# Optimization experiments

Hardware: AMD Instinct MI355X
Metric: run time of the kernel (lower is better)

## Reference

```python
import jax, jax.numpy as jnp
import numpy as np

N_NODES = 50000
N_EDGES = 800000
IN_CH = 256
OUT_CH = 128


def setup_inputs() -> dict:
    key = jax.random.key(0)
    k1, k2, k3, k4, k5, k6 = jax.random.split(key, 6)
    x = jax.random.normal(k1, (N_NODES, IN_CH), dtype=jnp.float32)
    edge_rows = jax.random.randint(k2, (N_EDGES,), 0, N_NODES, dtype=jnp.int64)
    edge_cols = jax.random.randint(k3, (N_EDGES,), 0, N_NODES, dtype=jnp.int64)
    # positive edge weights, roughly like a normalized adjacency (~1/degree)
    edge_vals = jax.random.uniform(k4, (N_EDGES,), dtype=jnp.float32) / 16.0
    # xavier_uniform: bound = sqrt(6/(fan_in+fan_out))
    bound = float(np.sqrt(6.0 / (IN_CH + OUT_CH)))
    weight = jax.random.uniform(k5, (IN_CH, OUT_CH), dtype=jnp.float32, minval=-bound, maxval=bound)
    gate_weight = jax.random.uniform(k6, (IN_CH, OUT_CH), dtype=jnp.float32, minval=-bound, maxval=bound)
    return {"x": x, "edge_rows": edge_rows, "edge_cols": edge_cols,
            "edge_vals": edge_vals, "weight": weight, "gate_weight": gate_weight}


def _spmm(edge_rows, edge_cols, edge_vals, dense, n_rows):
    # out[r] = sum over edges (r, c, v): v * dense[c]
    gathered = edge_vals[:, None] * dense[edge_cols]  # [E, out_ch]
    return jax.ops.segment_sum(gathered, edge_rows, num_segments=n_rows)


def reference(x, edge_rows, edge_cols, edge_vals, weight, gate_weight):
    support = x @ weight          # [N, out_ch]
    gate = x @ gate_weight        # [N, out_ch]
    n = x.shape[0]
    agg_support = _spmm(edge_rows, edge_cols, edge_vals, support, n)
    agg_gate = _spmm(edge_rows, edge_cols, edge_vals, gate, n)
    return jax.nn.sigmoid(agg_gate) * agg_support
```

## Files before the change

kernel.cpp:

```cpp
#include <hip/hip_runtime.h>
#include <hip/hip_bf16.h>

#define IN_CH 256
#define OUT_CH 128
#define NCAT 256
#define CAP 64
#define RPB 128
#define BINCAP 3072
#define EPB 4096

typedef __attribute__((ext_vector_type(8))) short bf16x8;
typedef __attribute__((ext_vector_type(4))) float f32x4;

__device__ __forceinline__ unsigned short f2bf(float f) {
  unsigned int u = __builtin_bit_cast(unsigned int, f);
  u += 0x7FFFu + ((u >> 16) & 1u);
  return (unsigned short)(u >> 16);
}
__device__ __forceinline__ unsigned int pack2bf(float a, float b) {
  return (unsigned int)f2bf(a) | ((unsigned int)f2bf(b) << 16);
}
__device__ __forceinline__ float bflo(unsigned int u) {
  return __builtin_bit_cast(float, u << 16);
}
__device__ __forceinline__ float bfhi(unsigned int u) {
  return __builtin_bit_cast(float, u & 0xFFFF0000u);
}

__global__ __launch_bounds__(256) void init_wcat(
    const float* __restrict__ w, const float* __restrict__ gw,
    unsigned short* __restrict__ wcat2, int* __restrict__ coarse_cnt,
    int nbins) {
  const int b = blockIdx.x;
  if (b < 256) {
    const int c = b;
    const int k = threadIdx.x;
    const int wc = c >> 6, s = c & 63, n = s >> 4, lr = s & 15;
    const int ch = 32 * wc + (n & 1) * 16 + lr;
    const float v = (n < 2) ? w[(size_t)k * 128 + ch]
                            : gw[(size_t)k * 128 + ch];
    wcat2[(size_t)c * 256 + k] = f2bf(v);
  } else {
    for (int j = threadIdx.x; j < nbins; j += 256) coarse_cnt[j] = 0;
  }
}

#define AST 80

__global__ __launch_bounds__(256) void gemm_and_bin(
    const float* __restrict__ x, const unsigned short* __restrict__ wcat2,
    char* __restrict__ comb, int nrows,
    const int* __restrict__ er, const int* __restrict__ ec,
    const float* __restrict__ ev, int* __restrict__ coarse_cnt,
    unsigned* __restrict__ cA, unsigned char* __restrict__ cB,
    int E, int nbins, int binBlocks) {
  __shared__ char smem[64 * AST + 256 * AST];

  if (blockIdx.x < binBlocks) {
    int* scnt = (int*)smem;
    int* sbase = (int*)smem + 512;
    const int t = threadIdx.x;
    const int e0 = blockIdx.x * EPB;

    for (int j = t; j < 512; j += 256) scnt[j] = 0;
    __syncthreads();

    int myr[16];
#pragma unroll
    for (int i = 0; i < 16; ++i) {
      const int e = e0 + i * 256 + t;
      int r = -1;
      if (e < E) { r = er[e]; atomicAdd(&scnt[r >> 7], 1); }
      myr[i] = r;
    }
    __syncthreads();

    for (int j = t; j < nbins; j += 256)
      sbase[j] = (scnt[j] > 0) ? atomicAdd(&coarse_cnt[j], scnt[j]) : 0;
    __syncthreads();
    for (int j = t; j < 512; j += 256) scnt[j] = 0;
    __syncthreads();

#pragma unroll
    for (int i = 0; i < 16; ++i) {
      const int r = myr[i];
      if (r >= 0) {
        const int e = e0 + i * 256 + t;
        const int b = r >> 7;
        const int idx = sbase[b] + atomicAdd(&scnt[b], 1);
        if (idx < BINCAP) {
          const size_t g = (size_t)b * BINCAP + idx;
          cA[g] = ((unsigned)ec[e] << 16) | (unsigned)f2bf(ev[e]);
          cB[g] = (unsigned char)(r & (RPB - 1));
        }
      }
    }
    return;
  }

  char* As = smem;
  char* Bs = smem + 64 * AST;
  const int t = threadIdx.x;
  const int lane = t & 63;
  const int wc = t >> 6;
  const int lrow = lane & 15;
  const int klane = lane >> 4;
  const int blockRow = (blockIdx.x - binBlocks) * 64;

  f32x4 acc[4][4];
#pragma unroll
  for (int m = 0; m < 4; ++m)
#pragma unroll
    for (int n = 0; n < 4; ++n) acc[m][n] = (f32x4){0.f, 0.f, 0.f, 0.f};

  const int arow = t >> 2;
  const int aseg = t & 3;
  const int agrow = blockRow + arow;
  const bool aok = (agrow < nrows);
  const float* xrow = x + (size_t)agrow * IN_CH + aseg * 8;
  const char* bsrc0 = (const char*)wcat2 + (size_t)t * 512;

  for (int kt = 0; kt < IN_CH; kt += 32) {
    {
      float4 v0 = make_float4(0, 0, 0, 0), v1 = v0;
      if (aok) {
        v0 = *(const float4*)(xrow + kt);
        v1 = *(const float4*)(xrow + kt + 4);
      }
      uint4 pk;
      pk.x = pack2bf(v0.x, v0.y); pk.y = pack2bf(v0.z, v0.w);
      pk.z = pack2bf(v1.x, v1.y); pk.w = pack2bf(v1.z, v1.w);
      *(uint4*)(As + arow * AST + aseg * 16) = pk;
    }
    {
      const char* src = bsrc0 + kt * 2;
      char* dst = Bs + t * AST;
      *(uint4*)(dst + 0)  = *(const uint4*)(src + 0);
      *(uint4*)(dst + 16) = *(const uint4*)(src + 16);
      *(uint4*)(dst + 32) = *(const uint4*)(src + 32);
      *(uint4*)(dst + 48) = *(const uint4*)(src + 48);
    }
    __syncthreads();

    bf16x8 af[4], bfm[4];
#pragma unroll
    for (int m = 0; m < 4; ++m)
      af[m] = *(const bf16x8*)(As + (m * 16 + lrow) * AST + klane * 16);
#pragma unroll
    for (int n = 0; n < 4; ++n)
      bfm[n] = *(const bf16x8*)(Bs + (wc * 64 + n * 16 + lrow) * AST + klane * 16);
#pragma unroll
    for (int m = 0; m < 4; ++m)
#pragma unroll
      for (int n = 0; n < 4; ++n)
        acc[m][n] = __builtin_amdgcn_mfma_f32_16x16x32_bf16(af[m], bfm[n], acc[m][n], 0, 0, 0);
    __syncthreads();
  }

#pragma unroll
  for (int m = 0; m < 4; ++m) {
#pragma unroll
    for (int j = 0; j < 4; ++j) {
      const int grow = blockRow + m * 16 + klane * 4 + j;
      if (grow < nrows) {
        uint2 val;
        val.x = pack2bf(acc[m][0][j], acc[m][2][j]);
        val.y = pack2bf(acc[m][1][j], acc[m][3][j]);
        *(uint2*)(comb + (size_t)grow * 512 + wc * 128 + lrow * 8) = val;
      }
    }
  }
}

__global__ __launch_bounds__(256) void bin_fine(
    const int* __restrict__ coarse_cnt, const unsigned* __restrict__ cA,
    const unsigned char* __restrict__ cB, int* __restrict__ cnt,
    unsigned* __restrict__ bucket4, int nrows) {
  __shared__ unsigned fine[RPB * CAP];
  __shared__ int lcnt[RPB];
  const int t = threadIdx.x;
  const int b = blockIdx.x;
  const int r0 = b * RPB;

  for (int j = t; j < RPB; j += 256) lcnt[j] = 0;
  __syncthreads();

  const int nE = min(coarse_cnt[b], BINCAP);
  for (int i = t; i < nE; i += 256) {
    const unsigned a = cA[(size_t)b * BINCAP + i];
    const int rl = cB[(size_t)b * BINCAP + i];
    const int idx = atomicAdd(&lcnt[rl], 1);
    if (idx < CAP) fine[rl * CAP + idx] = a;
  }
  __syncthreads();

  if (t < RPB && r0 + t < nrows) cnt[r0 + t] = min(lcnt[t], CAP);

  for (int s = t; s < RPB * CAP; s += 256) {
    const int rl = s >> 6;
    const int sl = s & 63;
    if (sl < min(lcnt[rl], CAP) && r0 + rl < nrows)
      bucket4[(size_t)(r0 + rl) * CAP + sl] = fine[s];
  }
}

__global__ __launch_bounds__(256) void spmm_fused(
    const unsigned* __restrict__ bucket4, const int* __restrict__ cnt,
    const char* __restrict__ comb, float* __restrict__ out, int nrows) {
  const int wid = (int)((blockIdx.x * 256 + threadIdx.x) >> 6);
  const int lane = threadIdx.x & 63;
  if (wid >= nrows) return;

  const int deg = min(cnt[wid], CAP);
  float s1 = 0.f, g1 = 0.f, s2 = 0.f, g2 = 0.f;

  if (deg > 0) {
    const unsigned my = bucket4[(size_t)wid * CAP + lane];
    for (int d = 0; d < deg; d += 8) {
      unsigned cj[8]; float vj[8]; uint2 q[8];
#pragma unroll
      for (int j = 0; j < 8; ++j) {
        const int dj = d + j;
        const int ds = dj < deg ? dj : deg - 1;
        const unsigned ent = (unsigned)__shfl((int)my, ds);
        cj[j] = ent >> 16;
        vj[j] = (dj < deg) ? bflo(ent) : 0.f;
      }
#pragma unroll
      for (int j = 0; j < 8; ++j)
        q[j] = *(const uint2*)(comb + (size_t)cj[j] * 512 + lane * 8);
#pragma unroll
      for (int j = 0; j < 8; ++j) {
        s1 += vj[j] * bflo(q[j].x);  g1 += vj[j] * bfhi(q[j].x);
        s2 += vj[j] * bflo(q[j].y);  g2 += vj[j] * bfhi(q[j].y);
      }
    }
  }
  const int gg = lane >> 4, lr = lane & 15;
  const int c1 = 32 * gg + lr;
  const float o1 = s1 / (1.f + __expf(-g1));
  const float o2 = s2 / (1.f + __expf(-g2));
  out[(size_t)wid * OUT_CH + c1]      = o1;
  out[(size_t)wid * OUT_CH + c1 + 16] = o2;
}

extern "C" void kernel_launch(void* const* d_in, const int* in_sizes, int n_in,
                              void* d_out, int out_size, void* d_ws, size_t ws_size,
                              hipStream_t stream) {
  const float* x  = (const float*)d_in[0];
  const int*   er = (const int*)d_in[1];
  const int*   ec = (const int*)d_in[2];
  const float* ev = (const float*)d_in[3];
  const float* w  = (const float*)d_in[4];
  const float* gw = (const float*)d_in[5];
  float* out = (float*)d_out;

  const int N = in_sizes[0] / IN_CH;
  const int E = in_sizes[1];
  const int nbins = (N + RPB - 1) / RPB;

  char* ws = (char*)d_ws;
  char* comb = ws;
  size_t off = (size_t)N * 512;
  unsigned short* wcat2 = (unsigned short*)(ws + off);  off += 256 * 256 * 2;
  int* cnt = (int*)(ws + off);                          off += ((size_t)N * 4 + 255) & ~255ull;
  unsigned* bucket4 = (unsigned*)(ws + off);            off += (size_t)N * CAP * 4;
  int* coarse_cnt = (int*)(ws + off);                   off += ((size_t)nbins * 4 + 255) & ~255ull;
  unsigned* cA = (unsigned*)(ws + off);                 off += (size_t)nbins * BINCAP * 4;
  unsigned char* cB = (unsigned char*)(ws + off);

  init_wcat<<<257, 256, 0, stream>>>(w, gw, wcat2, coarse_cnt, nbins);

  const int binBlocks = (E + EPB - 1) / EPB;
  const int gemmBlocks = (N + 63) / 64;
  gemm_and_bin<<<binBlocks + gemmBlocks, 256, 0, stream>>>(
      x, wcat2, comb, N, er, ec, ev, coarse_cnt, cA, cB, E, nbins, binBlocks);

  bin_fine<<<nbins, 256, 0, stream>>>(coarse_cnt, cA, cB, cnt, bucket4, N);

  const int blocks = (N + 3) / 4;
  spmm_fused<<<blocks, 256, 0, stream>>>(bucket4, cnt, comb, out, N);
}
```

Baseline: 109.7 us.

## Replace global-atomic coarse binning with per-block sorted segments and metadata

Each binning block now counting-sorts its 4096 edges by row bin in shared memory and writes a contiguous segment plus per-bin offset/count metadata, instead of reserving space in global bins with global atomics. The fine-binning kernel gathers each bin's pieces from all binning blocks, using a prefix scan and a binary search to map edge index to its source block. This removes the global atomics, the coarse counter zeroing, and the fixed bin capacity with its overflow drop. In exchange it adds scattered reads across about 196 segments per bin and a hardcoded NBIN that ties the code to the node count.

Measured after the change: 105.3 us. -4.1%, faster.

```diff
diff --git a/kernel.cpp b/kernel.cpp
--- a/kernel.cpp
+++ b/kernel.cpp
@@ -3,11 +3,11 @@
 
 #define IN_CH 256
 #define OUT_CH 128
-#define NCAT 256
 #define CAP 64
 #define RPB 128
-#define BINCAP 3072
 #define EPB 4096
+#define NBIN 392
+#define METAST 400
 
 typedef __attribute__((ext_vector_type(8))) short bf16x8;
 typedef __attribute__((ext_vector_type(4))) float f32x4;
@@ -29,20 +29,14 @@
 
 __global__ __launch_bounds__(256) void init_wcat(
     const float* __restrict__ w, const float* __restrict__ gw,
-    unsigned short* __restrict__ wcat2, int* __restrict__ coarse_cnt,
-    int nbins) {
-  const int b = blockIdx.x;
-  if (b < 256) {
-    const int c = b;
-    const int k = threadIdx.x;
-    const int wc = c >> 6, s = c & 63, n = s >> 4, lr = s & 15;
-    const int ch = 32 * wc + (n & 1) * 16 + lr;
-    const float v = (n < 2) ? w[(size_t)k * 128 + ch]
-                            : gw[(size_t)k * 128 + ch];
-    wcat2[(size_t)c * 256 + k] = f2bf(v);
-  } else {
-    for (int j = threadIdx.x; j < nbins; j += 256) coarse_cnt[j] = 0;
-  }
+    unsigned short* __restrict__ wcat2) {
+  const int c = blockIdx.x;
+  const int k = threadIdx.x;
+  const int wc = c >> 6, s = c & 63, n = s >> 4, lr = s & 15;
+  const int ch = 32 * wc + (n & 1) * 16 + lr;
+  const float v = (n < 2) ? w[(size_t)k * 128 + ch]
+                          : gw[(size_t)k * 128 + ch];
+  wcat2[(size_t)c * 256 + k] = f2bf(v);
 }
 
 #define AST 80
@@ -51,18 +45,20 @@
     const float* __restrict__ x, const unsigned short* __restrict__ wcat2,
     char* __restrict__ comb, int nrows,
     const int* __restrict__ er, const int* __restrict__ ec,
-    const float* __restrict__ ev, int* __restrict__ coarse_cnt,
-    unsigned* __restrict__ cA, unsigned char* __restrict__ cB,
-    int E, int nbins, int binBlocks) {
-  __shared__ char smem[64 * AST + 256 * AST];
+    const float* __restrict__ ev, uint2* __restrict__ seg,
+    unsigned* __restrict__ meta, int E, int binBlocks) {
+  __shared__ char smem[37728];
 
   if (blockIdx.x < binBlocks) {
-    int* scnt = (int*)smem;
-    int* sbase = (int*)smem + 512;
+    uint2* image = (uint2*)smem;
+    int* hist = (int*)(smem + 32768);
+    int* offs = (int*)(smem + 32768 + 1568);
+    int* cur  = (int*)(smem + 32768 + 3136);
+    int* gsum = (int*)(smem + 32768 + 4704);
     const int t = threadIdx.x;
     const int e0 = blockIdx.x * EPB;
 
-    for (int j = t; j < 512; j += 256) scnt[j] = 0;
+    for (int j = t; j < NBIN; j += 256) hist[j] = 0;
     __syncthreads();
 
     int myr[16];
@@ -70,15 +66,35 @@
     for (int i = 0; i < 16; ++i) {
       const int e = e0 + i * 256 + t;
       int r = -1;
-      if (e < E) { r = er[e]; atomicAdd(&scnt[r >> 7], 1); }
+      if (e < E) { r = er[e]; atomicAdd(&hist[r >> 7], 1); }
       myr[i] = r;
     }
     __syncthreads();
 
-    for (int j = t; j < nbins; j += 256)
-      sbase[j] = (scnt[j] > 0) ? atomicAdd(&coarse_cnt[j], scnt[j]) : 0;
-    __syncthreads();
-    for (int j = t; j < 512; j += 256) scnt[j] = 0;
+    if (t < 49) {
+      int s = 0;
+#pragma unroll
+      for (int k2 = 0; k2 < 8; ++k2) {
+        const int j = t * 8 + k2;
+        if (j < NBIN) { cur[j] = s; s += hist[j]; }
+      }
+      gsum[t] = s;
+    }
+    __syncthreads();
+    if (t == 0) {
+      int s = 0;
+      for (int b2 = 0; b2 < 49; ++b2) { const int g = gsum[b2]; gsum[b2] = s; s += g; }
+    }
+    __syncthreads();
+    if (t < 49) {
+#pragma unroll
+      for (int k2 = 0; k2 < 8; ++k2) {
+        const int j = t * 8 + k2;
+        if (j < NBIN) offs[j] = cur[j] + gsum[t];
+      }
+    }
+    __syncthreads();
+    for (int j = t; j < NBIN; j += 256) cur[j] = offs[j];
     __syncthreads();
 
 #pragma unroll
@@ -86,15 +102,19 @@
       const int r = myr[i];
       if (r >= 0) {
         const int e = e0 + i * 256 + t;
-        const int b = r >> 7;
-        const int idx = sbase[b] + atomicAdd(&scnt[b], 1);
-        if (idx < BINCAP) {
-          const size_t g = (size_t)b * BINCAP + idx;
-          cA[g] = ((unsigned)ec[e] << 16) | (unsigned)f2bf(ev[e]);
-          cB[g] = (unsigned char)(r & (RPB - 1));
-        }
-      }
-    }
+        const int b2 = r >> 7;
+        const int idx = atomicAdd(&cur[b2], 1);
+        image[idx] = make_uint2(((unsigned)ec[e] << 16) | (unsigned)f2bf(ev[e]),
+                                (unsigned)(r & (RPB - 1)));
+      }
+    }
+    __syncthreads();
+
+    uint2* segb = seg + (size_t)blockIdx.x * EPB;
+    for (int s2 = t; s2 < EPB; s2 += 256) segb[s2] = image[s2];
+    unsigned* metab = meta + (size_t)blockIdx.x * METAST;
+    for (int j = t; j < NBIN - 1; j += 256)
+      metab[j] = (unsigned)offs[j] | ((unsigned)hist[j] << 16);
     return;
   }
 
@@ -172,25 +192,54 @@
   }
 }
 
-__global__ __launch_bounds__(256) void bin_fine(
-    const int* __restrict__ coarse_cnt, const unsigned* __restrict__ cA,
-    const unsigned char* __restrict__ cB, int* __restrict__ cnt,
-    unsigned* __restrict__ bucket4, int nrows) {
+__global__ __launch_bounds__(256) void bin_fine2(
+    const uint2* __restrict__ seg, const unsigned* __restrict__ meta,
+    int* __restrict__ cnt, unsigned* __restrict__ bucket4,
+    int nrows, int nblk) {
   __shared__ unsigned fine[RPB * CAP];
   __shared__ int lcnt[RPB];
+  __shared__ int roff[224];
+  __shared__ int S[224];
+  __shared__ int Pex[225];
   const int t = threadIdx.x;
-  const int b = blockIdx.x;
-  const int r0 = b * RPB;
-
-  for (int j = t; j < RPB; j += 256) lcnt[j] = 0;
+  const int j = blockIdx.x;
+  const int r0 = j * RPB;
+
+  for (int k = t; k < RPB; k += 256) lcnt[k] = 0;
+  if (t < 224) {
+    if (t < nblk) {
+      const unsigned m = meta[(size_t)t * METAST + j];
+      roff[t] = (int)(m & 0xFFFFu);
+      S[t] = (int)(m >> 16);
+    } else {
+      S[t] = 0;
+    }
+  }
   __syncthreads();
 
-  const int nE = min(coarse_cnt[b], BINCAP);
-  for (int i = t; i < nE; i += 256) {
-    const unsigned a = cA[(size_t)b * BINCAP + i];
-    const int rl = cB[(size_t)b * BINCAP + i];
+  for (int d = 1; d < 224; d <<= 1) {
+    int v = 0;
+    if (t < 224 && t >= d) v = S[t - d];
+    __syncthreads();
+    if (t < 224) S[t] += v;
+    __syncthreads();
+  }
+  if (t == 0) Pex[0] = 0;
+  if (t < 224) Pex[t + 1] = S[t];
+  __syncthreads();
+
+  const int nE = Pex[nblk];
+  for (int e = t; e < nE; e += 256) {
+    int lo = 0, hi = nblk - 1;
+    while (lo < hi) {
+      const int mid = (lo + hi + 1) >> 1;
+      if (Pex[mid] <= e) lo = mid; else hi = mid - 1;
+    }
+    const int i = e - Pex[lo];
+    const uint2 ent = seg[(size_t)lo * EPB + roff[lo] + i];
+    const int rl = (int)ent.y;
     const int idx = atomicAdd(&lcnt[rl], 1);
-    if (idx < CAP) fine[rl * CAP + idx] = a;
+    if (idx < CAP) fine[rl * CAP + idx] = ent.x;
   }
   __syncthreads();
 
@@ -258,6 +307,7 @@
   const int N = in_sizes[0] / IN_CH;
   const int E = in_sizes[1];
   const int nbins = (N + RPB - 1) / RPB;
+  const int binBlocks = (E + EPB - 1) / EPB;
 
   char* ws = (char*)d_ws;
   char* comb = ws;
@@ -265,18 +315,16 @@
   unsigned short* wcat2 = (unsigned short*)(ws + off);  off += 256 * 256 * 2;
   int* cnt = (int*)(ws + off);                          off += ((size_t)N * 4 + 255) & ~255ull;
   unsigned* bucket4 = (unsigned*)(ws + off);            off += (size_t)N * CAP * 4;
-  int* coarse_cnt = (int*)(ws + off);                   off += ((size_t)nbins * 4 + 255) & ~255ull;
-  unsigned* cA = (unsigned*)(ws + off);                 off += (size_t)nbins * BINCAP * 4;
-  unsigned char* cB = (unsigned char*)(ws + off);
-
-  init_wcat<<<257, 256, 0, stream>>>(w, gw, wcat2, coarse_cnt, nbins);
-
-  const int binBlocks = (E + EPB - 1) / EPB;
+  uint2* seg = (uint2*)(ws + off);                      off += (size_t)binBlocks * EPB * 8;
+  unsigned* meta = (unsigned*)(ws + off);
+
+  init_wcat<<<256, 256, 0, stream>>>(w, gw, wcat2);
+
   const int gemmBlocks = (N + 63) / 64;
   gemm_and_bin<<<binBlocks + gemmBlocks, 256, 0, stream>>>(
-      x, wcat2, comb, N, er, ec, ev, coarse_cnt, cA, cB, E, nbins, binBlocks);
-
-  bin_fine<<<nbins, 256, 0, stream>>>(coarse_cnt, cA, cB, cnt, bucket4, N);
+      x, wcat2, comb, N, er, ec, ev, seg, meta, E, binBlocks);
+
+  bin_fine2<<<nbins, 256, 0, stream>>>(seg, meta, cnt, bucket4, N, binBlocks);
 
   const int blocks = (N + 3) / 4;
   spmm_fused<<<blocks, 256, 0, stream>>>(bucket4, cnt, comb, out, N);
```
